# Kernel optimization log

Hardware: AMD Instinct MI355X
Metric: run time of the kernel (lower is better)

Reference implementation:

```python
import jax, jax.numpy as jnp
import numpy as np

B, N, D, U = 8, 2048, 512, 512

def setup_inputs() -> dict:
    key = jax.random.key(0)
    ks = jax.random.split(key, 7)
    s = 1.0 / np.sqrt(D)
    return {
        "inputs": jax.random.normal(ks[0], (B, N, D), dtype=jnp.float32),
        "Wq": jax.random.normal(ks[1], (D, U), dtype=jnp.float32) * s,
        "bq": jnp.zeros((U,), dtype=jnp.float32),
        "Wk": jax.random.normal(ks[2], (D, U), dtype=jnp.float32) * s,
        "bk": jnp.zeros((U,), dtype=jnp.float32),
        "Wv": jax.random.normal(ks[3], (D, U), dtype=jnp.float32) * s,
        "bv": jnp.zeros((U,), dtype=jnp.float32),
    }

def reference(inputs, Wq, bq, Wk, bk, Wv, bv):
    # Dense projections (Keras Dense: x @ W + b)
    Q = inputs @ Wq + bq  # [B, N, U]
    K = inputs @ Wk + bk  # [B, N, U]
    V = inputs @ Wv + bv  # [B, N, U]
    # NOTE: original module has NO 1/sqrt(d) scaling
    scores = jnp.einsum("bnu,bmu->bnm", Q, K)  # [B, N, N]
    attn = jax.nn.softmax(scores, axis=-1)
    return jnp.einsum("bnm,bmu->bnu", attn, V)  # [B, N, U]
```

## Files before the change

### kernel.cpp

```cpp
#include <hip/hip_runtime.h>


typedef _Float16 f16;
typedef _Float16 f16x4 __attribute__((ext_vector_type(4)));
typedef _Float16 f16x8 __attribute__((ext_vector_type(8)));
typedef float f32x4 __attribute__((ext_vector_type(4)));
typedef short s16x8 __attribute__((ext_vector_type(8)));
typedef unsigned short u16;

#define OFS 96.0f

__device__ __forceinline__ void stage16(const void* g, void* lds_uniform) {
    __builtin_amdgcn_global_load_lds(
        (const __attribute__((address_space(1))) void*)g,
        (__attribute__((address_space(3))) void*)lds_uniform,
        16, 0, 0);
}

__device__ __forceinline__ u16 f2bf(float f) {
    unsigned u = __builtin_bit_cast(unsigned, f);
    u = (u + 0x7FFF + ((u >> 16) & 1)) >> 16;
    return (u16)u;
}
__device__ __forceinline__ float bf2f(u16 b) {
    return __builtin_bit_cast(float, (unsigned)b << 16);
}

__global__ __launch_bounds__(256) void prep_fused(
    const float* __restrict__ X,
    const float* __restrict__ Wq, const float* __restrict__ Wk,
    const float* __restrict__ Wv,
    const float* __restrict__ bq, const float* __restrict__ bk,
    const float* __restrict__ bv,
    f16* __restrict__ X16, f16* __restrict__ Wt, float* __restrict__ biases,
    float* __restrict__ rowsum) {
    __shared__ float t[32][33];
    const int bid = blockIdx.x, tid = threadIdx.x;
    if (bid < 8192) {
        int i = (bid * 256 + tid) * 4;
        float4 v = *(const float4*)(X + i);
        f16x4 o;
        o[0] = (f16)v.x; o[1] = (f16)v.y; o[2] = (f16)v.z; o[3] = (f16)v.w;
        *(f16x4*)(X16 + i) = o;
    } else if (bid < 8960) {
        int id = bid - 8192;
        int z = id >> 8, rem = id & 255;
        int u0 = (rem & 15) * 32, d0 = (rem >> 4) * 32;
        const float* W = (z == 0) ? Wq : (z == 1 ? Wk : Wv);
        f16* outp = Wt + (size_t)z * 262144;
        int tx = tid & 31, ty = tid >> 5;
#pragma unroll
        for (int r = 0; r < 4; r++)
            t[ty + 8 * r][tx] = W[(size_t)(d0 + ty + 8 * r) * 512 + u0 + tx];
        __syncthreads();
#pragma unroll
        for (int r = 0; r < 4; r++)
            outp[(size_t)(u0 + ty + 8 * r) * 512 + d0 + tx] = (f16)t[tx][ty + 8 * r];
    } else if (bid == 8960) {
#pragma unroll
        for (int j = 0; j < 6; j++) {
            int i = j * 256 + tid;
            float v = (i < 512) ? bq[i] : (i < 1024) ? bk[i - 512] : bv[i - 1024];
            biases[i] = v;
        }
    } else {
        int id = bid - 8961;
        float4 z4 = {0.f, 0.f, 0.f, 0.f};
        ((float4*)rowsum)[id * 256 + tid] = z4;
    }
}

template <int MODE>
__device__ __forceinline__ void gemm_core(
    const u16* __restrict__ A, int lda,
    const u16* __restrict__ Bt, int ldb,
    int m0, int n0, int K,
    const float* __restrict__ bias, float* __restrict__ rs,
    void* __restrict__ Cv, int ldc,
    u16* As, u16* Bs) {
    __shared__ float rowbuf[128];

    const int tid = threadIdx.x;
    const int wid = tid >> 6, lane = tid & 63;

    if (MODE == 2 || MODE == 4) {
        if (tid < 128) rowbuf[tid] = (MODE == 2 ? bias : rs)[m0 + tid];
    }

    const int schunk = (lane & 7) ^ ((lane >> 3) & 7);
    const u16* gA = A + (size_t)(m0 + wid * 32 + (lane >> 3)) * lda + schunk * 8;
    const u16* gB = Bt + (size_t)(n0 + wid * 32 + (lane >> 3)) * ldb + schunk * 8;
    u16* ldsA = As + (wid * 32) * 64;
    u16* ldsB = Bs + (wid * 32) * 64;

    const int wr = wid >> 1, wc = wid & 1;
    const int frow = lane & 15;
    const int f7 = frow & 7;
    const int c_lo = (lane >> 4) ^ f7;
    const int c_hi = ((lane >> 4) | 4) ^ f7;
    const u16* fA_lo = As + (wr * 64 + frow) * 64 + c_lo * 8;
    const u16* fA_hi = As + (wr * 64 + frow) * 64 + c_hi * 8;
    const u16* fB_lo = Bs + (wc * 64 + frow) * 64 + c_lo * 8;
    const u16* fB_hi = Bs + (wc * 64 + frow) * 64 + c_hi * 8;

    f32x4 acc[4][4] = {};

    for (int kt = 0; kt < K; kt += 64) {
#pragma unroll
        for (int j = 0; j < 4; j++)
            stage16(gA + (size_t)(j * 8) * lda, ldsA + (j * 8) * 64);
#pragma unroll
        for (int j = 0; j < 4; j++)
            stage16(gB + (size_t)(j * 8) * ldb, ldsB + (j * 8) * 64);
        gA += 64; gB += 64;
        __syncthreads();

#pragma unroll
        for (int half = 0; half < 2; half++) {
            const u16* pA = half ? fA_hi : fA_lo;
            const u16* pB = half ? fB_hi : fB_lo;
            if (MODE == 4) {
                s16x8 af[4], bf[4];
#pragma unroll
                for (int i = 0; i < 4; i++) af[i] = *(const s16x8*)(pA + i * 16 * 64);
#pragma unroll
                for (int i = 0; i < 4; i++) bf[i] = *(const s16x8*)(pB + i * 16 * 64);
#pragma unroll
                for (int mi = 0; mi < 4; mi++)
#pragma unroll
                    for (int ni = 0; ni < 4; ni++)
                        acc[mi][ni] = __builtin_amdgcn_mfma_f32_16x16x32_bf16(
                            af[mi], bf[ni], acc[mi][ni], 0, 0, 0);
            } else {
                f16x8 af[4], bf[4];
#pragma unroll
                for (int i = 0; i < 4; i++) af[i] = *(const f16x8*)(const f16*)(pA + i * 16 * 64);
#pragma unroll
                for (int i = 0; i < 4; i++) bf[i] = *(const f16x8*)(const f16*)(pB + i * 16 * 64);
#pragma unroll
                for (int mi = 0; mi < 4; mi++)
#pragma unroll
                    for (int ni = 0; ni < 4; ni++)
                        acc[mi][ni] = __builtin_amdgcn_mfma_f32_16x16x32_f16(
                            af[mi], bf[ni], acc[mi][ni], 0, 0, 0);
            }
        }
        __syncthreads();
    }

    const int crow0 = m0 + wr * 64 + ((lane >> 4) << 2);
    const int ccol0 = n0 + wc * 64 + (lane & 15);

    if (MODE == 1) {
        f16* C = (f16*)Cv;
#pragma unroll
        for (int mi = 0; mi < 4; mi++)
#pragma unroll
            for (int ni = 0; ni < 4; ni++) {
                float cb = bias[ccol0 + ni * 16];
#pragma unroll
                for (int r = 0; r < 4; r++)
                    C[(size_t)(crow0 + mi * 16 + r) * ldc + ccol0 + ni * 16] =
                        (f16)(acc[mi][ni][r] + cb);
            }
    } else if (MODE == 2) {
        u16* C = (u16*)Cv;
#pragma unroll
        for (int mi = 0; mi < 4; mi++)
#pragma unroll
            for (int ni = 0; ni < 4; ni++)
#pragma unroll
                for (int r = 0; r < 4; r++) {
                    float rb = rowbuf[crow0 + mi * 16 + r - m0];
                    C[(size_t)(crow0 + mi * 16 + r) * ldc + ccol0 + ni * 16] =
                        f2bf(acc[mi][ni][r] + rb);
                }
    } else {
        float* C = (float*)Cv;
#pragma unroll
        for (int mi = 0; mi < 4; mi++) {
            float inv[4];
#pragma unroll
            for (int r = 0; r < 4; r++)
                inv[r] = 1.0f / rowbuf[crow0 + mi * 16 + r - m0];
#pragma unroll
            for (int ni = 0; ni < 4; ni++)
#pragma unroll
                for (int r = 0; r < 4; r++)
                    C[(size_t)(crow0 + mi * 16 + r) * ldc + ccol0 + ni * 16] =
                        acc[mi][ni][r] * inv[r];
        }
    }
}

__global__ __launch_bounds__(256) void proj_fused(
    const u16* __restrict__ X16, const u16* __restrict__ Wt,
    const float* __restrict__ biases,
    u16* __restrict__ QK, u16* __restrict__ Vt) {
    __shared__ __align__(16) u16 As[128 * 64];
    __shared__ __align__(16) u16 Bs[128 * 64];
    const int bid = blockIdx.x;
    if (bid < 1024) {
        int z = bid >> 9, rem = bid & 511;
        int bx = rem & 127, by = rem >> 7;
        gemm_core<1>(X16, 512, Wt + (size_t)z * 262144, 512,
                     bx * 128, by * 128, 512,
                     biases + z * 512, nullptr,
                     QK + (size_t)z * 8388608, 512, As, Bs);
    } else {
        int id = bid - 1024;
        int bz = id & 7, rem = id >> 3;
        int bx = rem & 3, by = rem >> 2;
        gemm_core<2>(Wt + (size_t)2 * 262144, 512,
                     X16 + (size_t)bz * 1048576, 512,
                     bx * 128, by * 128, 512,
                     biases + 1024, nullptr,
                     Vt + (size_t)bz * 1048576, 2048, As, Bs);
    }
}

__global__ __launch_bounds__(512, 2) void score_gemm(
    const u16* __restrict__ Q, const u16* __restrict__ Kk,
    u16* __restrict__ P, float* __restrict__ rowsum) {
    extern __shared__ __align__(16) char smem[];
    u16* As = (u16*)smem;
    u16* Bs = (u16*)(smem + 65536);

    const int i = blockIdx.x;
    const int z = i & 7, y = (i >> 3) & 7, x = i >> 6;
    const int m0 = x * 256, n0 = y * 256;
    const u16* A = Q + (size_t)z * 1048576;
    const u16* Bt = Kk + (size_t)z * 1048576;
    u16* C = P + (size_t)z * 4194304;
    float* rs = rowsum + z * 2048;

    const int tid = threadIdx.x;
    const int wid = tid >> 6, lane = tid & 63;

    const int schunk = (lane & 7) ^ ((lane >> 3) & 7);
    const u16* gA = A + (size_t)(m0 + wid * 32 + (lane >> 3)) * 512 + schunk * 8;
    const u16* gB = Bt + (size_t)(n0 + wid * 32 + (lane >> 3)) * 512 + schunk * 8;
    const int ldsOff = (wid * 32) * 64;

    const int wr = wid >> 2, wc = wid & 3;
    const int frow = lane & 15;
    const int f7 = frow & 7;
    const int c_lo = (lane >> 4) ^ f7;
    const int c_hi = ((lane >> 4) | 4) ^ f7;
    const int offA_lo = (wr * 128 + frow) * 64 + c_lo * 8;
    const int offA_hi = (wr * 128 + frow) * 64 + c_hi * 8;
    const int offB_lo = (wc * 64 + frow) * 64 + c_lo * 8;
    const int offB_hi = (wc * 64 + frow) * 64 + c_hi * 8;

    f32x4 acc[8][4] = {};

    auto compute = [&](int buf) {
        const u16* baseA = As + buf * 16384;
        const u16* baseB = Bs + buf * 16384;
#pragma unroll
        for (int half = 0; half < 2; half++) {
            const u16* pA = baseA + (half ? offA_hi : offA_lo);
            const u16* pB = baseB + (half ? offB_hi : offB_lo);
            f16x8 bf[4];
#pragma unroll
            for (int ni = 0; ni < 4; ni++)
                bf[ni] = *(const f16x8*)(const f16*)(pB + ni * 16 * 64);
#pragma unroll
            for (int mig = 0; mig < 2; mig++) {
                f16x8 af[4];
#pragma unroll
                for (int j = 0; j < 4; j++)
                    af[j] = *(const f16x8*)(const f16*)(pA + ((mig * 4 + j) * 16) * 64);
#pragma unroll
                for (int j = 0; j < 4; j++)
#pragma unroll
                    for (int ni = 0; ni < 4; ni++)
                        acc[mig * 4 + j][ni] = __builtin_amdgcn_mfma_f32_16x16x32_f16(
                            af[j], bf[ni], acc[mig * 4 + j][ni], 0, 0, 0);
            }
        }
    };

#pragma unroll
    for (int j = 0; j < 4; j++)
        stage16(gA + (size_t)(j * 8) * 512, As + ldsOff + (j * 8) * 64);
#pragma unroll
    for (int j = 0; j < 4; j++)
        stage16(gB + (size_t)(j * 8) * 512, Bs + ldsOff + (j * 8) * 64);
    gA += 64; gB += 64;
    __syncthreads();

    int cur = 0;
    for (int kt = 1; kt < 8; ++kt) {
        u16* a1 = As + (cur ^ 1) * 16384 + ldsOff;
        u16* b1 = Bs + (cur ^ 1) * 16384 + ldsOff;
#pragma unroll
        for (int j = 0; j < 4; j++)
            stage16(gA + (size_t)(j * 8) * 512, a1 + (j * 8) * 64);
#pragma unroll
        for (int j = 0; j < 4; j++)
            stage16(gB + (size_t)(j * 8) * 512, b1 + (j * 8) * 64);
        gA += 64; gB += 64;

        compute(cur);
        __syncthreads();
        cur ^= 1;
    }
    compute(cur);

    const int crow0 = m0 + wr * 128 + ((lane >> 4) << 2);
    const int ccol0 = n0 + wc * 64 + (lane & 15);
#pragma unroll
    for (int mi = 0; mi < 8; mi++)
#pragma unroll
        for (int r = 0; r < 4; r++) {
            float rsum = 0.0f;
#pragma unroll
            for (int ni = 0; ni < 4; ni++) {
                u16 b = f2bf(__expf(acc[mi][ni][r] - OFS));
                C[(size_t)(crow0 + mi * 16 + r) * 2048 + ccol0 + ni * 16] = b;
                rsum += bf2f(b);
            }
#pragma unroll
            for (int o = 1; o < 16; o <<= 1)
                rsum += __shfl_xor(rsum, o, 64);
            if ((lane & 15) == 0)
                atomicAdd(rs + crow0 + mi * 16 + r, rsum);
        }
}

__global__ __launch_bounds__(256) void pv_gemm(
    const u16* __restrict__ P, const u16* __restrict__ Vt,
    float* __restrict__ rowsum, float* __restrict__ out) {
    __shared__ __align__(16) u16 As[128 * 64];
    __shared__ __align__(16) u16 Bs[128 * 64];
    const int i = blockIdx.x;
    const int z = i & 7, y = (i >> 3) & 3, x = i >> 5;
    gemm_core<4>(P + (size_t)z * 4194304, 2048,
                 Vt + (size_t)z * 1048576, 2048,
                 x * 128, y * 128, 2048,
                 nullptr, rowsum + z * 2048,
                 out + (size_t)z * 1048576, 512, As, Bs);
}


extern "C" void kernel_launch(void* const* d_in, const int* in_sizes, int n_in,
                              void* d_out, int out_size, void* d_ws, size_t ws_size,
                              hipStream_t stream) {
    const float* X  = (const float*)d_in[0];
    const float* Wq = (const float*)d_in[1];
    const float* bq = (const float*)d_in[2];
    const float* Wk = (const float*)d_in[3];
    const float* bk = (const float*)d_in[4];
    const float* Wv = (const float*)d_in[5];
    const float* bv = (const float*)d_in[6];
    float* out = (float*)d_out;
    char* ws = (char*)d_ws;

    f16*   X16    = (f16*)ws;
    f16*   Wt     = (f16*)(ws + 16777216);
    float* biases = (float*)(ws + 18350080);
    u16*   QK     = (u16*)(ws + 18356224);
    u16*   Vt     = (u16*)(ws + 51910656);
    u16*   P      = (u16*)(ws + 68687872);
    float* rowsum = (float*)(ws + 135796736);

    static bool s_attr_done = false;
    if (!s_attr_done) {
        (void)hipFuncSetAttribute(reinterpret_cast<const void*>(score_gemm),
                                  hipFuncAttributeMaxDynamicSharedMemorySize,
                                  131072);
        s_attr_done = true;
    }

    prep_fused<<<8977, 256, 0, stream>>>(X, Wq, Wk, Wv, bq, bk, bv,
                                         X16, Wt, biases, rowsum);

    proj_fused<<<1536, 256, 0, stream>>>((const u16*)X16, (const u16*)Wt,
                                         biases, QK, Vt);

    score_gemm<<<512, 512, 131072, stream>>>(QK, QK + (size_t)8388608, P, rowsum);

    pv_gemm<<<512, 256, 0, stream>>>(P, Vt, rowsum, out);
}
```

Before: 217.4 us.

## Interleave fine-grained LDS staging with MFMA phases in score GEMM

Restructures the score GEMM main loop into four sub-phases per K-tile. Each phase loads a slice of A fragments, issues one staging unit of the next tiles, and runs MFMAs at raised wave priority, separated by raw s_barriers and explicit vmcnt waits. Loads are spread across phases, with prefetch up to two tiles ahead into the buffer being consumed, so that global-to-LDS traffic overlaps compute instead of arriving in bursts before a __syncthreads. The hand-placed barriers and wait counts are fragile, and a wrong count would race on the shared buffers.

Measured after the change: 220.4 us. About the same (+1.4%).

```diff
diff --git a/kernel.cpp b/kernel.cpp
--- a/kernel.cpp
+++ b/kernel.cpp
@@ -229,7 +229,7 @@
     const int i = blockIdx.x;
     const int z = i & 7, y = (i >> 3) & 7, x = i >> 6;
     const int m0 = x * 256, n0 = y * 256;
-    const u16* A = Q + (size_t)z * 1048576;
+    const u16* A  = Q  + (size_t)z * 1048576;
     const u16* Bt = Kk + (size_t)z * 1048576;
     u16* C = P + (size_t)z * 4194304;
     float* rs = rowsum + z * 2048;
@@ -237,76 +237,104 @@
     const int tid = threadIdx.x;
     const int wid = tid >> 6, lane = tid & 63;
 
-    const int schunk = (lane & 7) ^ ((lane >> 3) & 7);
-    const u16* gA = A + (size_t)(m0 + wid * 32 + (lane >> 3)) * 512 + schunk * 8;
-    const u16* gB = Bt + (size_t)(n0 + wid * 32 + (lane >> 3)) * 512 + schunk * 8;
-    const int ldsOff = (wid * 32) * 64;
+    const int srow = lane >> 3;
+    const int schunk = (lane & 7) ^ srow;
+    const u16* gA0 = A  + (size_t)m0 * 512 + schunk * 8;
+    const u16* gB0 = Bt + (size_t)n0 * 512 + schunk * 8;
+    const int w16 = wid * 16;
+    const int baseU2 = w16 + (wid >= 4 ? 64 : 0);
+
+    auto stage_unit = [&](int u, int T, int b) {
+        int base = (u == 0) ? w16
+                 : (u == 1) ? 128 + w16
+                 : (u == 2) ? baseU2
+                 : 64 + baseU2;
+        const u16* g = (u < 2 ? gB0 : gA0) + (size_t)(base + srow) * 512 + T * 64;
+        u16* l = (u < 2 ? Bs : As) + b * 16384 + base * 64;
+        stage16(g, l);
+        stage16(g + (size_t)8 * 512, l + 8 * 64);
+    };
 
     const int wr = wid >> 2, wc = wid & 3;
     const int frow = lane & 15;
     const int f7 = frow & 7;
     const int c_lo = (lane >> 4) ^ f7;
     const int c_hi = ((lane >> 4) | 4) ^ f7;
+    const int offB_lo = (wc * 64 + frow) * 64 + c_lo * 8;
+    const int offB_hi = (wc * 64 + frow) * 64 + c_hi * 8;
     const int offA_lo = (wr * 128 + frow) * 64 + c_lo * 8;
     const int offA_hi = (wr * 128 + frow) * 64 + c_hi * 8;
-    const int offB_lo = (wc * 64 + frow) * 64 + c_lo * 8;
-    const int offB_hi = (wc * 64 + frow) * 64 + c_hi * 8;
 
     f32x4 acc[8][4] = {};
 
-    auto compute = [&](int buf) {
-        const u16* baseA = As + buf * 16384;
-        const u16* baseB = Bs + buf * 16384;
-#pragma unroll
-        for (int half = 0; half < 2; half++) {
-            const u16* pA = baseA + (half ? offA_hi : offA_lo);
-            const u16* pB = baseB + (half ? offB_hi : offB_lo);
-            f16x8 bf[4];
-#pragma unroll
-            for (int ni = 0; ni < 4; ni++)
-                bf[ni] = *(const f16x8*)(const f16*)(pB + ni * 16 * 64);
-#pragma unroll
-            for (int mig = 0; mig < 2; mig++) {
-                f16x8 af[4];
-#pragma unroll
-                for (int j = 0; j < 4; j++)
-                    af[j] = *(const f16x8*)(const f16*)(pA + ((mig * 4 + j) * 16) * 64);
-#pragma unroll
-                for (int j = 0; j < 4; j++)
+    stage_unit(0, 0, 0); stage_unit(1, 0, 0);
+    stage_unit(2, 0, 0); stage_unit(3, 0, 0);
+    stage_unit(0, 1, 1); stage_unit(1, 1, 1); stage_unit(2, 1, 1);
+    asm volatile("s_waitcnt vmcnt(6)" ::: "memory");
+    asm volatile("s_barrier" ::: "memory");
+
+#pragma unroll 2
+    for (int T = 0; T < 8; ++T) {
+        const int buf = T & 1;
+        const u16* Ab = As + buf * 16384;
+        const u16* Bb = Bs + buf * 16384;
+
+        f16x8 bf[4][2];
+        {
+#pragma unroll
+            for (int ni = 0; ni < 4; ni++) {
+                bf[ni][0] = *(const f16x8*)(const f16*)(Bb + offB_lo + ni * 16 * 64);
+                bf[ni][1] = *(const f16x8*)(const f16*)(Bb + offB_hi + ni * 16 * 64);
+            }
+            f16x8 af[2][2];
+#pragma unroll
+            for (int m2 = 0; m2 < 2; m2++) {
+                af[m2][0] = *(const f16x8*)(const f16*)(Ab + offA_lo + m2 * 16 * 64);
+                af[m2][1] = *(const f16x8*)(const f16*)(Ab + offA_hi + m2 * 16 * 64);
+            }
+            if (T < 7) stage_unit(3, T + 1, buf ^ 1);
+            asm volatile("s_barrier" ::: "memory");
+            asm volatile("s_waitcnt lgkmcnt(0)" ::: "memory");
+            __builtin_amdgcn_s_setprio(1);
+#pragma unroll
+            for (int kh = 0; kh < 2; kh++)
+#pragma unroll
+                for (int m2 = 0; m2 < 2; m2++)
 #pragma unroll
                     for (int ni = 0; ni < 4; ni++)
-                        acc[mig * 4 + j][ni] = __builtin_amdgcn_mfma_f32_16x16x32_f16(
-                            af[j], bf[ni], acc[mig * 4 + j][ni], 0, 0, 0);
-            }
-        }
-    };
-
-#pragma unroll
-    for (int j = 0; j < 4; j++)
-        stage16(gA + (size_t)(j * 8) * 512, As + ldsOff + (j * 8) * 64);
-#pragma unroll
-    for (int j = 0; j < 4; j++)
-        stage16(gB + (size_t)(j * 8) * 512, Bs + ldsOff + (j * 8) * 64);
-    gA += 64; gB += 64;
-    __syncthreads();
-
-    int cur = 0;
-    for (int kt = 1; kt < 8; ++kt) {
-        u16* a1 = As + (cur ^ 1) * 16384 + ldsOff;
-        u16* b1 = Bs + (cur ^ 1) * 16384 + ldsOff;
-#pragma unroll
-        for (int j = 0; j < 4; j++)
-            stage16(gA + (size_t)(j * 8) * 512, a1 + (j * 8) * 64);
-#pragma unroll
-        for (int j = 0; j < 4; j++)
-            stage16(gB + (size_t)(j * 8) * 512, b1 + (j * 8) * 64);
-        gA += 64; gB += 64;
-
-        compute(cur);
-        __syncthreads();
-        cur ^= 1;
-    }
-    compute(cur);
+                        acc[m2][ni] = __builtin_amdgcn_mfma_f32_16x16x32_f16(
+                            af[m2][kh], bf[ni][kh], acc[m2][ni], 0, 0, 0);
+            __builtin_amdgcn_s_setprio(0);
+            asm volatile("s_barrier" ::: "memory");
+        }
+#pragma unroll
+        for (int q = 1; q < 4; q++) {
+            f16x8 af[2][2];
+#pragma unroll
+            for (int m2 = 0; m2 < 2; m2++) {
+                af[m2][0] = *(const f16x8*)(const f16*)(Ab + offA_lo + (q * 2 + m2) * 16 * 64);
+                af[m2][1] = *(const f16x8*)(const f16*)(Ab + offA_hi + (q * 2 + m2) * 16 * 64);
+            }
+            if (T < 6) stage_unit(q - 1, T + 2, buf);
+            asm volatile("s_barrier" ::: "memory");
+            asm volatile("s_waitcnt lgkmcnt(0)" ::: "memory");
+            __builtin_amdgcn_s_setprio(1);
+#pragma unroll
+            for (int kh = 0; kh < 2; kh++)
+#pragma unroll
+                for (int m2 = 0; m2 < 2; m2++)
+#pragma unroll
+                    for (int ni = 0; ni < 4; ni++)
+                        acc[q * 2 + m2][ni] = __builtin_amdgcn_mfma_f32_16x16x32_f16(
+                            af[m2][kh], bf[ni][kh], acc[q * 2 + m2][ni], 0, 0, 0);
+            __builtin_amdgcn_s_setprio(0);
+            if (q == 3) {
+                if (T < 6)       asm volatile("s_waitcnt vmcnt(6)" ::: "memory");
+                else if (T == 6) asm volatile("s_waitcnt vmcnt(0)" ::: "memory");
+            }
+            asm volatile("s_barrier" ::: "memory");
+        }
+    }
 
     const int crow0 = m0 + wr * 128 + ((lane >> 4) << 2);
     const int ccol0 = n0 + wc * 64 + (lane & 15);
```
